# Kernel optimization log

Hardware: AMD Instinct MI355X
Metric: run time of the kernel (lower is better)

Reference implementation:

```python
import jax, jax.numpy as jnp
import numpy as np

N = 50000      # nodes
E = 800000     # edges (avg degree 16)
D = 128        # in_dim
H = 128        # hidden_dim
C = 10         # n_classes
G = 128        # graphs in batch
N_HID = 3      # hidden_layers (total convs = 1 + N_HID)


def setup_inputs() -> dict:
    key = jax.random.key(0)
    ks = jax.random.split(key, 10)
    s = 0.05  # weight init scale
    x = jax.random.normal(ks[0], (N, D), jnp.float32)
    edge_index = jax.random.randint(ks[1], (2, E), 0, N, dtype=jnp.int32)
    graph_ids = jnp.sort(jax.random.randint(ks[2], (N,), 0, G, dtype=jnp.int32))
    W0 = jax.random.normal(ks[3], (D, H), jnp.float32) * s
    b0 = jnp.zeros((H,), jnp.float32)
    Ws = jax.random.normal(ks[4], (N_HID, H, H), jnp.float32) * s
    bs = jnp.zeros((N_HID, H), jnp.float32)
    Wc = jax.random.normal(ks[5], (H, C), jnp.float32) * s
    bc = jnp.zeros((C,), jnp.float32)
    return {"x": x, "W0": W0, "b0": b0, "Ws": Ws, "bs": bs,
            "Wc": Wc, "bc": bc, "edge_index": edge_index, "graph_ids": graph_ids}


def reference(x, W0, b0, Ws, bs, Wc, bc, edge_index, graph_ids):
    src, dst = edge_index[0], edge_index[1]
    ones_e = jnp.ones((E,), x.dtype)
    # DGL GraphConv norm='both': D_out^{-1/2} on source side, D_in^{-1/2} on dest side
    out_deg = jax.ops.segment_sum(ones_e, src, num_segments=N)
    in_deg = jax.ops.segment_sum(ones_e, dst, num_segments=N)
    c_src = jnp.clip(out_deg, 1.0) ** -0.5  # [N]
    c_dst = jnp.clip(in_deg, 1.0) ** -0.5   # [N]

    def conv(h, W, b):
        # h' = relu( c_dst * A (c_src * h) W + b ); dropout is identity in eval mode
        h = h * c_src[:, None]
        m = jax.ops.segment_sum(h[src], dst, num_segments=N)  # gather + scatter-add
        m = m * c_dst[:, None]
        return jax.nn.relu(m @ W + b)

    h = conv(x, W0, b0)
    for i in range(N_HID):  # fixed small layer count
        h = conv(h, Ws[i], bs[i])

    # mean readout per graph
    cnt = jax.ops.segment_sum(jnp.ones((N,), h.dtype), graph_ids, num_segments=G)
    hg = jax.ops.segment_sum(h, graph_ids, num_segments=G) / jnp.clip(cnt, 1.0)[:, None]
    return hg @ Wc + bc  # [G, C]
```

## Files before the change

kernel.cpp:

```cpp
#include <hip/hip_runtime.h>

#define N_NODES 50000
#define N_EDGES 800000
#define DIM     128
#define NGRAPH  128
#define NCLASS  10
#define NLAYER  4

#define TEAMS   256
#define ESLICE  (N_EDGES / TEAMS)
#define CWORDS  12500
#define DUMMY   50000

#define SCAT_B  256
#define PRE_B   3126
#define W_B     8
#define Z_B     17

typedef __attribute__((ext_vector_type(8))) short short8;
typedef __attribute__((ext_vector_type(4))) float floatx4;

__device__ __forceinline__ unsigned f2bf(float f) {
    union { float f; unsigned u; } v; v.f = f;
    return (v.u + 0x7fffu + ((v.u >> 16) & 1u)) >> 16;
}
__device__ __forceinline__ float bf_lo(unsigned u) { return __uint_as_float(u << 16); }
__device__ __forceinline__ float bf_hi(unsigned u) { return __uint_as_float(u & 0xffff0000u); }

__global__ __launch_bounds__(1024) void count_kernel(
    const int* __restrict__ ei, unsigned* __restrict__ cntw,
    unsigned* __restrict__ colc_fill)
{
    __shared__ unsigned h[CWORDS];
    int team = blockIdx.x, tid = threadIdx.x;
    for (int i = tid; i < CWORDS; i += 1024) h[i] = 0;
    __syncthreads();
    const int e0 = team * ESLICE;
    const int* __restrict__ srcp = ei;
    const int* __restrict__ dstp = ei + N_EDGES;
    for (int e = e0 + tid; e < e0 + ESLICE; e += 1024) {
        int s = srcp[e], d = dstp[e];
        atomicAdd(&h[d >> 2], 1u  << (8 * (d & 3)));
        atomicAdd(&h[s >> 2], 16u << (8 * (s & 3)));
    }
    __syncthreads();
    for (int i = tid; i < CWORDS; i += 1024)
        cntw[(size_t)team * CWORDS + i] = h[i];
    for (int i = blockIdx.x * 1024 + tid; i < N_NODES * 32; i += TEAMS * 1024)
        colc_fill[i] = 0xC350C350u;
}

__global__ __launch_bounds__(1024) void offsets_kernel(
    const unsigned* __restrict__ cntw, unsigned* __restrict__ offsw,
    unsigned* __restrict__ cnt_dense, float* __restrict__ c_src,
    float* __restrict__ c_dst)
{
    __shared__ unsigned ldsC[128 * 64];
    __shared__ unsigned ldsO[128 * 64];
    __shared__ unsigned totG[4 * 256];
    __shared__ unsigned baseW[4 * 64];
    int tid = threadIdx.x;
    int g = tid >> 8;
    int n = tid & 255;
    int n0 = blockIdx.x * 256;
    int w0 = n0 >> 2;
    unsigned carryIn = 0, carryOut = 0;
    for (int ph = 0; ph < 2; ++ph) {
        int t0 = ph * 128;
        for (int i = tid; i < 128 * 64; i += 1024) {
            int tl = i >> 6, wl = i & 63;
            int gw = w0 + wl;
            ldsC[i] = (gw < CWORDS) ? cntw[(size_t)(t0 + tl) * CWORDS + gw] : 0u;
        }
        __syncthreads();
        unsigned locIn = 0, locOut = 0;
        {
            unsigned char* ob = (unsigned char*)ldsO;
            for (int tl = g * 32; tl < g * 32 + 32; ++tl) {
                unsigned wvd = ldsC[tl * 64 + (n >> 2)];
                unsigned b = (wvd >> (8 * (n & 3))) & 255u;
                ob[tl * 256 + n] = (unsigned char)locIn;
                locIn  += (b & 15u);
                locOut += (b >> 4);
            }
        }
        totG[g * 256 + n] = locIn | (locOut << 16);
        __syncthreads();
        unsigned baseIn = 0, sumIn = 0, sumOut = 0;
#pragma unroll
        for (int gg = 0; gg < 4; ++gg) {
            unsigned t = totG[gg * 256 + n];
            if (gg < g) baseIn += (t & 0xffffu);
            sumIn += (t & 0xffffu); sumOut += (t >> 16);
        }
        ((unsigned char*)baseW)[g * 256 + n] = (unsigned char)(carryIn + baseIn);
        carryIn += sumIn; carryOut += sumOut;
        __syncthreads();
        for (int i = tid; i < 128 * 64; i += 1024) {
            int tl = i >> 6, wl = i & 63;
            int gw = w0 + wl;
            if (gw < CWORDS)
                offsw[(size_t)(t0 + tl) * CWORDS + gw] =
                    ldsO[i] + baseW[(tl >> 5) * 64 + wl];
        }
        __syncthreads();
    }
    if (tid < 256) {
        int nn = n0 + tid;
        if (nn < N_NODES) {
            unsigned id_ = carryIn, od = carryOut;
            cnt_dense[nn] = id_ > 64u ? 64u : id_;
            if (id_ < 1u) id_ = 1u;
            if (od < 1u) od = 1u;
            c_dst[nn] = 1.0f / sqrtf((float)id_);
            c_src[nn] = 1.0f / sqrtf((float)od);
        }
    }
}

__global__ __launch_bounds__(1024) void sp_kernel(
    const int* __restrict__ ei, const unsigned* __restrict__ offsw,
    unsigned short* __restrict__ colc,
    const float2* __restrict__ x, const float* __restrict__ c_src,
    unsigned* __restrict__ hsA, unsigned* __restrict__ hsB,
    const float* __restrict__ W0, const float* __restrict__ Ws,
    uint4* __restrict__ Wf, float* __restrict__ hg, float* __restrict__ cntg)
{
    __shared__ unsigned h[CWORDS];
    int bid = blockIdx.x, tid = threadIdx.x;
    if (bid < SCAT_B) {
        int team = bid;
        for (int i = tid; i < CWORDS; i += 1024) h[i] = 0;
        __syncthreads();
        const unsigned char* __restrict__ ob =
            (const unsigned char*)offsw + (size_t)team * 50000;
        const int e0 = team * ESLICE;
        const int* __restrict__ srcp = ei;
        const int* __restrict__ dstp = ei + N_EDGES;
        for (int e = e0 + tid; e < e0 + ESLICE; e += 1024) {
            int s = srcp[e], d = dstp[e];
            unsigned old = atomicAdd(&h[d >> 2], 1u << (8 * (d & 3)));
            unsigned pos = (old >> (8 * (d & 3))) & 15u;
            unsigned slot = (unsigned)ob[d] + pos;
            if (slot < 64u) colc[(size_t)d * 64 + slot] = (unsigned short)s;
        }
        return;
    }
    if (bid < SCAT_B + PRE_B) {
        int i = (bid - SCAT_B) * 1024 + tid;
        if (i >= (N_NODES + 1) * 64) return;
        int row = i >> 6;
        if (row < N_NODES) {
            float c = c_src[row];
            float2 v = x[i];
            hsA[i] = f2bf(v.x * c) | (f2bf(v.y * c) << 16);
        } else {
            hsA[i] = 0u;
            hsB[i] = 0u;
        }
        return;
    }
    if (bid < SCAT_B + PRE_B + W_B) {
        int t = (bid - SCAT_B - PRE_B) * 1024 + tid;
        if (t >= NLAYER * 2048) return;
        int layer = t >> 11;
        int rem = t & 2047;
        int lane = rem & 63;
        int s = (rem >> 6) & 3;
        int c = rem >> 8;
        int quad = lane >> 4, colw = c * 16 + (lane & 15);
        int k0 = s * 32 + quad * 8;
        const float* W = (layer == 0) ? W0 : Ws + (size_t)(layer - 1) * DIM * DIM;
        uint4 p;
        unsigned* pp = (unsigned*)&p;
#pragma unroll
        for (int j = 0; j < 4; ++j) {
            unsigned lo = f2bf(W[(size_t)(k0 + 2 * j) * DIM + colw]);
            unsigned hi = f2bf(W[(size_t)(k0 + 2 * j + 1) * DIM + colw]);
            pp[j] = lo | (hi << 16);
        }
        Wf[t] = p;
        return;
    }
    int idx = (bid - SCAT_B - PRE_B - W_B) * 1024 + tid;
    if (idx < NGRAPH * DIM) hg[idx] = 0.f;
    else if (idx < NGRAPH * DIM + NGRAPH) cntg[idx - NGRAPH * DIM] = 0.f;
}

__global__ __launch_bounds__(256) void layer_kernel(
    const unsigned* __restrict__ hs, const unsigned short* __restrict__ colc,
    const unsigned* __restrict__ cnt_dense, const uint4* __restrict__ Wf,
    const float* __restrict__ bias, const float* __restrict__ c_dst,
    const float* __restrict__ c_src, unsigned short* __restrict__ out_bf,
    float* __restrict__ out_f32, int last)
{
    __shared__ unsigned Ash[16 * 64];
    char* Ab = (char*)Ash;
    int tid = threadIdx.x;
    int lane = tid & 63;
    int wv = __builtin_amdgcn_readfirstlane(tid >> 6);
    int r0 = blockIdx.x * 16;
    int nb = r0 + wv * 4;
    const unsigned* __restrict__ cw = (const unsigned*)colc;
    const char* __restrict__ hb = (const char*)hs;
    unsigned loff = (unsigned)(lane << 2);

    unsigned dg0 = cnt_dense[nb + 0], dg1 = cnt_dense[nb + 1];
    unsigned dg2 = cnt_dense[nb + 2], dg3 = cnt_dense[nb + 3];
    unsigned m01 = dg0 > dg1 ? dg0 : dg1, m23 = dg2 > dg3 ? dg2 : dg3;
    unsigned mx = m01 > m23 ? m01 : m23;
    unsigned row0 = cw[(unsigned)(nb + 0) * 32u + (unsigned)(lane & 31)];
    unsigned row1 = cw[(unsigned)(nb + 1) * 32u + (unsigned)(lane & 31)];
    unsigned row2 = cw[(unsigned)(nb + 2) * 32u + (unsigned)(lane & 31)];
    unsigned row3 = cw[(unsigned)(nb + 3) * 32u + (unsigned)(lane & 31)];

    float f00 = 0.f, f01 = 0.f, f10 = 0.f, f11 = 0.f;
    float f20 = 0.f, f21 = 0.f, f30 = 0.f, f31 = 0.f;
    for (unsigned j = 0; j < mx; j += 8) {
#pragma unroll
        for (int k = 0; k < 4; ++k) {
            int sl = (int)(j >> 1) + k;
            unsigned w0 = (unsigned)__builtin_amdgcn_readlane((int)row0, sl);
            unsigned w1 = (unsigned)__builtin_amdgcn_readlane((int)row1, sl);
            unsigned w2 = (unsigned)__builtin_amdgcn_readlane((int)row2, sl);
            unsigned w3 = (unsigned)__builtin_amdgcn_readlane((int)row3, sl);
            unsigned u00 = *(const unsigned*)(hb + ((w0 & 0xffffu) << 8) + loff);
            unsigned u01 = *(const unsigned*)(hb + ((w0 >> 16) << 8) + loff);
            unsigned u10 = *(const unsigned*)(hb + ((w1 & 0xffffu) << 8) + loff);
            unsigned u11 = *(const unsigned*)(hb + ((w1 >> 16) << 8) + loff);
            unsigned u20 = *(const unsigned*)(hb + ((w2 & 0xffffu) << 8) + loff);
            unsigned u21 = *(const unsigned*)(hb + ((w2 >> 16) << 8) + loff);
            unsigned u30 = *(const unsigned*)(hb + ((w3 & 0xffffu) << 8) + loff);
            unsigned u31 = *(const unsigned*)(hb + ((w3 >> 16) << 8) + loff);
            f00 += bf_lo(u00); f01 += bf_hi(u00);
            f00 += bf_lo(u01); f01 += bf_hi(u01);
            f10 += bf_lo(u10); f11 += bf_hi(u10);
            f10 += bf_lo(u11); f11 += bf_hi(u11);
            f20 += bf_lo(u20); f21 += bf_hi(u20);
            f20 += bf_lo(u21); f21 += bf_hi(u21);
            f30 += bf_lo(u30); f31 += bf_hi(u30);
            f30 += bf_lo(u31); f31 += bf_hi(u31);
        }
    }
    {
        int il = wv * 4;
        *(unsigned*)(Ab + il * 256 + ((lane << 2) ^ ((il & 7) << 4))) =
            f2bf(f00) | (f2bf(f01) << 16);
        il++;
        *(unsigned*)(Ab + il * 256 + ((lane << 2) ^ ((il & 7) << 4))) =
            f2bf(f10) | (f2bf(f11) << 16);
        il++;
        *(unsigned*)(Ab + il * 256 + ((lane << 2) ^ ((il & 7) << 4))) =
            f2bf(f20) | (f2bf(f21) << 16);
        il++;
        *(unsigned*)(Ab + il * 256 + ((lane << 2) ^ ((il & 7) << 4))) =
            f2bf(f30) | (f2bf(f31) << 16);
    }
    __syncthreads();

    int quad = lane >> 4, m16 = lane & 15;
    union U { uint4 u; short8 s; };
    U a[4];
#pragma unroll
    for (int s = 0; s < 4; ++s)
        a[s].u = *(const uint4*)(
            Ab + m16 * 256 + ((s * 64 + quad * 16) ^ ((m16 & 7) << 4)));

    floatx4 acc[2];
#pragma unroll
    for (int cc = 0; cc < 2; ++cc) {
        int c = wv * 2 + cc;
        floatx4 ac = {0.f, 0.f, 0.f, 0.f};
#pragma unroll
        for (int s = 0; s < 4; ++s) {
            U b; b.u = Wf[(c * 4 + s) * 64 + lane];
            ac = __builtin_amdgcn_mfma_f32_16x16x32_bf16(a[s].s, b.s, ac, 0, 0, 0);
        }
        acc[cc] = ac;
    }

    float cd[4], cs[4];
#pragma unroll
    for (int r = 0; r < 4; ++r) {
        int row = r0 + quad * 4 + r;
        cd[r] = c_dst[row];
        cs[r] = last ? 1.f : c_src[row];
    }
#pragma unroll
    for (int cc = 0; cc < 2; ++cc) {
        int colg = (wv * 2 + cc) * 16 + m16;
        float b = bias[colg];
#pragma unroll
        for (int r = 0; r < 4; ++r) {
            int row = r0 + quad * 4 + r;
            float v = acc[cc][r] * cd[r] + b;
            v = v > 0.f ? v : 0.f;
            if (last) out_f32[(size_t)row * DIM + colg] = v;
            else      out_bf[(size_t)row * DIM + colg] = (unsigned short)f2bf(v * cs[r]);
        }
    }
}

__global__ __launch_bounds__(128) void readout_kernel(
    const float* __restrict__ h, const int* __restrict__ gid,
    float* __restrict__ hg, float* __restrict__ cntg)
{
    int j  = threadIdx.x;
    int n0 = blockIdx.x * 64;
    float acc = 0.f; int cur = -1; int run = 0;
    for (int i = 0; i < 64; ++i) {
        int n = n0 + i;
        if (n >= N_NODES) break;
        int g = gid[n];
        if (g != cur) {
            if (cur >= 0) {
                atomicAdd(&hg[cur * DIM + j], acc);
                if (j == 0) atomicAdd(&cntg[cur], (float)run);
            }
            cur = g; acc = 0.f; run = 0;
        }
        acc += h[(size_t)n * DIM + j];
        run++;
    }
    if (cur >= 0) {
        atomicAdd(&hg[cur * DIM + j], acc);
        if (j == 0) atomicAdd(&cntg[cur], (float)run);
    }
}

__global__ __launch_bounds__(256) void head_kernel(
    const float* __restrict__ hg, const float* __restrict__ cntg,
    const float* __restrict__ Wc, const float* __restrict__ bc,
    float* __restrict__ out)
{
    int idx = blockIdx.x * blockDim.x + threadIdx.x;
    if (idx >= NGRAPH * NCLASS) return;
    int g = idx / NCLASS, c = idx % NCLASS;
    float inv = 1.0f / fmaxf(cntg[g], 1.0f);
    float s = 0.f;
    for (int j = 0; j < DIM; ++j) s = fmaf(hg[g * DIM + j], Wc[j * NCLASS + c], s);
    out[idx] = s * inv + bc[c];
}

extern "C" void kernel_launch(void* const* d_in, const int* in_sizes, int n_in,
                              void* d_out, int out_size, void* d_ws, size_t ws_size,
                              hipStream_t stream)
{
    const float* x   = (const float*)d_in[0];
    const float* W0  = (const float*)d_in[1];
    const float* b0  = (const float*)d_in[2];
    const float* Ws  = (const float*)d_in[3];
    const float* bs  = (const float*)d_in[4];
    const float* Wc  = (const float*)d_in[5];
    const float* bc  = (const float*)d_in[6];
    const int*   ei  = (const int*)d_in[7];
    const int*   gid = (const int*)d_in[8];
    float* out = (float*)d_out;

    char* ws = (char*)d_ws;
    size_t o = 0;
    auto alloc = [&](size_t bytes) {
        size_t r = o; o = (o + bytes + 255) & ~(size_t)255; return r;
    };
    unsigned* cntw      = (unsigned*)(ws + alloc((size_t)TEAMS * CWORDS * 4));
    unsigned* offsw     = (unsigned*)(ws + alloc((size_t)TEAMS * CWORDS * 4));
    unsigned* cnt_dense = (unsigned*)(ws + alloc((size_t)N_NODES * 4));
    float*    c_src     = (float*)(ws + alloc((size_t)N_NODES * 4));
    float*    c_dst     = (float*)(ws + alloc((size_t)N_NODES * 4));
    unsigned short* colc = (unsigned short*)(ws + alloc((size_t)N_NODES * 64 * 2));
    unsigned* hsA       = (unsigned*)(ws + alloc((size_t)(N_NODES + 1) * 64 * 4));
    unsigned* hsB       = (unsigned*)(ws + alloc((size_t)(N_NODES + 1) * 64 * 4));
    float*    hlast     = (float*)(ws + alloc((size_t)N_NODES * DIM * 4));
    uint4*    Wf        = (uint4*)(ws + alloc((size_t)NLAYER * 2048 * 16));
    float*    hg        = (float*)(ws + alloc((size_t)NGRAPH * DIM * 4));
    float*    cntg      = (float*)(ws + alloc((size_t)NGRAPH * 4));

    count_kernel<<<TEAMS, 1024, 0, stream>>>(ei, cntw, (unsigned*)colc);
    offsets_kernel<<<(N_NODES + 255) / 256, 1024, 0, stream>>>(
        cntw, offsw, cnt_dense, c_src, c_dst);
    sp_kernel<<<SCAT_B + PRE_B + W_B + Z_B, 1024, 0, stream>>>(
        ei, offsw, colc, (const float2*)x, c_src, hsA, hsB, W0, Ws, Wf, hg, cntg);

    const int LAYER_BLOCKS = N_NODES / 16;

    for (int l = 0; l < NLAYER; ++l) {
        const float* b = (l == 0) ? b0 : (bs + (size_t)(l - 1) * DIM);
        int last = (l == NLAYER - 1) ? 1 : 0;
        const unsigned* hin = (l & 1) ? hsB : hsA;
        unsigned* hout      = (l & 1) ? hsA : hsB;
        layer_kernel<<<LAYER_BLOCKS, 256, 0, stream>>>(
            hin, colc, cnt_dense, Wf + (size_t)l * 2048, b, c_dst, c_src,
            (unsigned short*)hout, hlast, last);
    }

    readout_kernel<<<(N_NODES + 63) / 64, 128, 0, stream>>>(hlast, gid, hg, cntg);
    head_kernel<<<(NGRAPH * NCLASS + 255) / 256, 256, 0, stream>>>(hg, cntg, Wc, bc, out);
}
```

Before: 266.5 us.

## Fuse mean readout and classifier head into one per-graph kernel

Replaces the atomic-based readout kernel and the separate head kernel with a single kernel that runs one block per graph. Each block binary-searches the sorted graph ids for its node range, sums the node rows with a shared-memory reduction, and computes the class logits directly. This removes the zeroing of the accumulators, the global atomics and one launch. The risk is load imbalance, since only 128 blocks each stream roughly 400 rows, and the kernel relies on graph_ids being sorted.

```diff
diff --git a/kernel.cpp b/kernel.cpp
--- a/kernel.cpp
+++ b/kernel.cpp
@@ -15,7 +15,6 @@
 #define SCAT_B  256
 #define PRE_B   3126
 #define W_B     8
-#define Z_B     17
 
 typedef __attribute__((ext_vector_type(8))) short short8;
 typedef __attribute__((ext_vector_type(4))) float floatx4;
@@ -124,7 +123,7 @@
     const float2* __restrict__ x, const float* __restrict__ c_src,
     unsigned* __restrict__ hsA, unsigned* __restrict__ hsB,
     const float* __restrict__ W0, const float* __restrict__ Ws,
-    uint4* __restrict__ Wf, float* __restrict__ hg, float* __restrict__ cntg)
+    uint4* __restrict__ Wf)
 {
     __shared__ unsigned h[CWORDS];
     int bid = blockIdx.x, tid = threadIdx.x;
@@ -160,31 +159,25 @@
         }
         return;
     }
-    if (bid < SCAT_B + PRE_B + W_B) {
-        int t = (bid - SCAT_B - PRE_B) * 1024 + tid;
-        if (t >= NLAYER * 2048) return;
-        int layer = t >> 11;
-        int rem = t & 2047;
-        int lane = rem & 63;
-        int s = (rem >> 6) & 3;
-        int c = rem >> 8;
-        int quad = lane >> 4, colw = c * 16 + (lane & 15);
-        int k0 = s * 32 + quad * 8;
-        const float* W = (layer == 0) ? W0 : Ws + (size_t)(layer - 1) * DIM * DIM;
-        uint4 p;
-        unsigned* pp = (unsigned*)&p;
-#pragma unroll
-        for (int j = 0; j < 4; ++j) {
-            unsigned lo = f2bf(W[(size_t)(k0 + 2 * j) * DIM + colw]);
-            unsigned hi = f2bf(W[(size_t)(k0 + 2 * j + 1) * DIM + colw]);
-            pp[j] = lo | (hi << 16);
-        }
-        Wf[t] = p;
-        return;
-    }
-    int idx = (bid - SCAT_B - PRE_B - W_B) * 1024 + tid;
-    if (idx < NGRAPH * DIM) hg[idx] = 0.f;
-    else if (idx < NGRAPH * DIM + NGRAPH) cntg[idx - NGRAPH * DIM] = 0.f;
+    int t = (bid - SCAT_B - PRE_B) * 1024 + tid;
+    if (t >= NLAYER * 2048) return;
+    int layer = t >> 11;
+    int rem = t & 2047;
+    int lane = rem & 63;
+    int s = (rem >> 6) & 3;
+    int c = rem >> 8;
+    int quad = lane >> 4, colw = c * 16 + (lane & 15);
+    int k0 = s * 32 + quad * 8;
+    const float* W = (layer == 0) ? W0 : Ws + (size_t)(layer - 1) * DIM * DIM;
+    uint4 p;
+    unsigned* pp = (unsigned*)&p;
+#pragma unroll
+    for (int j = 0; j < 4; ++j) {
+        unsigned lo = f2bf(W[(size_t)(k0 + 2 * j) * DIM + colw]);
+        unsigned hi = f2bf(W[(size_t)(k0 + 2 * j + 1) * DIM + colw]);
+        pp[j] = lo | (hi << 16);
+    }
+    Wf[t] = p;
 }
 
 __global__ __launch_bounds__(256) void layer_kernel(
@@ -301,45 +294,40 @@
     }
 }
 
-__global__ __launch_bounds__(128) void readout_kernel(
+__global__ __launch_bounds__(512) void graph_kernel(
     const float* __restrict__ h, const int* __restrict__ gid,
-    float* __restrict__ hg, float* __restrict__ cntg)
-{
-    int j  = threadIdx.x;
-    int n0 = blockIdx.x * 64;
-    float acc = 0.f; int cur = -1; int run = 0;
-    for (int i = 0; i < 64; ++i) {
-        int n = n0 + i;
-        if (n >= N_NODES) break;
-        int g = gid[n];
-        if (g != cur) {
-            if (cur >= 0) {
-                atomicAdd(&hg[cur * DIM + j], acc);
-                if (j == 0) atomicAdd(&cntg[cur], (float)run);
-            }
-            cur = g; acc = 0.f; run = 0;
-        }
-        acc += h[(size_t)n * DIM + j];
-        run++;
-    }
-    if (cur >= 0) {
-        atomicAdd(&hg[cur * DIM + j], acc);
-        if (j == 0) atomicAdd(&cntg[cur], (float)run);
-    }
-}
-
-__global__ __launch_bounds__(256) void head_kernel(
-    const float* __restrict__ hg, const float* __restrict__ cntg,
     const float* __restrict__ Wc, const float* __restrict__ bc,
     float* __restrict__ out)
 {
-    int idx = blockIdx.x * blockDim.x + threadIdx.x;
-    if (idx >= NGRAPH * NCLASS) return;
-    int g = idx / NCLASS, c = idx % NCLASS;
-    float inv = 1.0f / fmaxf(cntg[g], 1.0f);
-    float s = 0.f;
-    for (int j = 0; j < DIM; ++j) s = fmaf(hg[g * DIM + j], Wc[j * NCLASS + c], s);
-    out[idx] = s * inv + bc[c];
+    __shared__ float part[512];
+    __shared__ float hgv[DIM];
+    int g = blockIdx.x;
+    int tid = threadIdx.x;
+    int lo = 0, hi = N_NODES;
+    while (lo < hi) { int mid = (lo + hi) >> 1; if (gid[mid] < g) lo = mid + 1; else hi = mid; }
+    int start = lo;
+    hi = N_NODES;
+    while (lo < hi) { int mid = (lo + hi) >> 1; if (gid[mid] < g + 1) lo = mid + 1; else hi = mid; }
+    int end = lo;
+
+    int j = tid & 127, q = tid >> 7;
+    float acc = 0.f;
+    for (int n = start + q; n < end; n += 4)
+        acc += h[(size_t)n * DIM + j];
+    part[tid] = acc;
+    __syncthreads();
+    if (tid < DIM) {
+        float s = part[tid] + part[tid + 128] + part[tid + 256] + part[tid + 384];
+        hgv[tid] = s / fmaxf((float)(end - start), 1.0f);
+    }
+    __syncthreads();
+    if (tid < NCLASS) {
+        float s = 0.f;
+#pragma unroll 8
+        for (int jj = 0; jj < DIM; ++jj)
+            s = fmaf(hgv[jj], Wc[jj * NCLASS + tid], s);
+        out[g * NCLASS + tid] = s + bc[tid];
+    }
 }
 
 extern "C" void kernel_launch(void* const* d_in, const int* in_sizes, int n_in,
@@ -372,14 +360,12 @@
     unsigned* hsB       = (unsigned*)(ws + alloc((size_t)(N_NODES + 1) * 64 * 4));
     float*    hlast     = (float*)(ws + alloc((size_t)N_NODES * DIM * 4));
     uint4*    Wf        = (uint4*)(ws + alloc((size_t)NLAYER * 2048 * 16));
-    float*    hg        = (float*)(ws + alloc((size_t)NGRAPH * DIM * 4));
-    float*    cntg      = (float*)(ws + alloc((size_t)NGRAPH * 4));
 
     count_kernel<<<TEAMS, 1024, 0, stream>>>(ei, cntw, (unsigned*)colc);
     offsets_kernel<<<(N_NODES + 255) / 256, 1024, 0, stream>>>(
         cntw, offsw, cnt_dense, c_src, c_dst);
-    sp_kernel<<<SCAT_B + PRE_B + W_B + Z_B, 1024, 0, stream>>>(
-        ei, offsw, colc, (const float2*)x, c_src, hsA, hsB, W0, Ws, Wf, hg, cntg);
+    sp_kernel<<<SCAT_B + PRE_B + W_B, 1024, 0, stream>>>(
+        ei, offsw, colc, (const float2*)x, c_src, hsA, hsB, W0, Ws, Wf);
 
     const int LAYER_BLOCKS = N_NODES / 16;
 
@@ -393,6 +379,5 @@
             (unsigned short*)hout, hlast, last);
     }
 
-    readout_kernel<<<(N_NODES + 63) / 64, 128, 0, stream>>>(hlast, gid, hg, cntg);
-    head_kernel<<<(NGRAPH * NCLASS + 255) / 256, 256, 0, stream>>>(hg, cntg, Wc, bc, out);
-}
+    graph_kernel<<<NGRAPH, 512, 0, stream>>>(hlast, gid, Wc, bc, out);
+}
```

After: 272.5 us. 2.2% more time.
